# Kernel tuning notes

Hardware: AMD Instinct MI355X
Metric: run time of the kernel (lower is better)

Reference implementation:

```python
import jax, jax.numpy as jnp
import numpy as np

B, S, H, NH, HD = 2, 2048, 1024, 16, 64
THETA = 10000.0


def setup_inputs() -> dict:
    key = jax.random.key(0)
    k1, k2, k3, k4, k5 = jax.random.split(key, 5)
    hidden_states = jax.random.normal(k1, (B, S, H), dtype=jnp.float32)
    # RoPE tables, interleaved-pair layout: [c0,c0,c1,c1,...] along head_dim
    inv_freq = 1.0 / (THETA ** (jnp.arange(0, HD, 2, dtype=jnp.float32) / HD))
    t = jnp.arange(S, dtype=jnp.float32)
    freqs = jnp.outer(t, inv_freq)                      # [S, HD//2]
    freqs_cos = jnp.repeat(jnp.cos(freqs), 2, axis=-1)  # [S, HD]
    freqs_sin = jnp.repeat(jnp.sin(freqs), 2, axis=-1)  # [S, HD]
    position_ids = jnp.arange(S, dtype=jnp.int32)
    w = 0.02
    Wq = jax.random.normal(k2, (H, H), dtype=jnp.float32) * w
    Wk = jax.random.normal(k3, (H, H), dtype=jnp.float32) * w
    Wv = jax.random.normal(k4, (H, H), dtype=jnp.float32) * w
    Wo = jax.random.normal(k5, (H, H), dtype=jnp.float32) * w
    return {"hidden_states": hidden_states, "freqs_cos": freqs_cos,
            "freqs_sin": freqs_sin, "position_ids": position_ids,
            "Wq": Wq, "Wk": Wk, "Wv": Wv, "Wo": Wo}


def _rotate_half_interleaved(x):
    # stack([-x[..., 1::2], x[..., ::2]], -1).reshape_as(x)
    xe = x.reshape(x.shape[:-1] + (HD // 2, 2))
    return jnp.stack([-xe[..., 1], xe[..., 0]], axis=-1).reshape(x.shape)


def reference(hidden_states, freqs_cos, freqs_sin, position_ids, Wq, Wk, Wv, Wo):
    b, s, _ = hidden_states.shape
    # QKV projections (torch Linear: y = x @ W.T), split into heads [b, nh, s, hd]
    q = jnp.einsum('bsh,oh->bso', hidden_states, Wq).reshape(b, s, NH, HD).transpose(0, 2, 1, 3)
    k = jnp.einsum('bsh,oh->bso', hidden_states, Wk).reshape(b, s, NH, HD).transpose(0, 2, 1, 3)
    v = jnp.einsum('bsh,oh->bso', hidden_states, Wv).reshape(b, s, NH, HD).transpose(0, 2, 1, 3)
    cos = freqs_cos[position_ids][None, None]  # [1, 1, s, hd]
    sin = freqs_sin[position_ids][None, None]
    rq = _rotate_half_interleaved(q)
    # NOTE: faithful to source bug — rotate_half_k is built from q, not k
    q = q * cos + rq * sin
    k = k * cos + rq * sin
    # causal SDPA, scale = 1/sqrt(head_dim)
    scores = jnp.einsum('bhqd,bhkd->bhqk', q, k) / jnp.sqrt(jnp.float32(HD))
    causal = jnp.tril(jnp.ones((s, s), dtype=bool))
    scores = jnp.where(causal, scores, jnp.float32(-1e30))
    attn = jax.nn.softmax(scores, axis=-1)
    out = jnp.einsum('bhqk,bhkd->bhqd', attn, v)
    out = out.transpose(0, 2, 1, 3).reshape(b, s, H)
    return jnp.einsum('bsh,oh->bso', out, Wo)
```

## Files before the change

### kernel.cpp

```cpp
#include <hip/hip_runtime.h>
#include <stdint.h>

#define BB 2
#define SS 2048
#define HH 1024
#define NHH 16
#define HDD 64

typedef short bf16s;
typedef __attribute__((ext_vector_type(8))) short short8;
typedef __attribute__((ext_vector_type(4))) short short4v;
typedef __attribute__((ext_vector_type(2))) short short2v;
typedef __attribute__((ext_vector_type(4))) float f32x4;
typedef _Float16 half4v __attribute__((ext_vector_type(4)));
typedef _Float16 half8v __attribute__((ext_vector_type(8)));
typedef __fp16 fp16x2 __attribute__((ext_vector_type(2)));

__device__ inline short f2bf(float f) {
  union { float f; uint32_t u; } v; v.f = f;
  uint32_t r = (v.u + 0x7fffu + ((v.u >> 16) & 1u)) >> 16;
  return (short)r;
}
__device__ inline float bf2f(short h) {
  union { uint32_t u; float f; } v; v.u = ((uint32_t)(uint16_t)h) << 16;
  return v.f;
}

__device__ __forceinline__ float exp2_raw(float x) {
  float r;
  asm("v_exp_f32 %0, %1\n\ts_nop 0" : "=v"(r) : "v"(x));
  return r;
}

__device__ inline void gld_lds16(const void* g, void* l) {
  __builtin_amdgcn_global_load_lds((const __attribute__((address_space(1))) void*)g,
                                   (__attribute__((address_space(3))) void*)l, 16, 0, 0);
}

__device__ inline void stv(short* C, size_t i, float v) { C[i] = f2bf(v); }
__device__ inline void stv(float* C, size_t i, float v) { C[i] = v; }

__device__ inline f32x4 mfma_k32(short8 a, short8 b, f32x4 c) {
  return __builtin_amdgcn_mfma_f32_16x16x32_bf16(a, b, c, 0, 0, 0);
}
__device__ inline f32x4 mfma_k32(half8v a, half8v b, f32x4 c) {
  return __builtin_amdgcn_mfma_f32_16x16x32_f16(a, b, c, 0, 0, 0);
}
template <typename ET> struct ftr;
template <> struct ftr<short>     { using v8 = short8; };
template <> struct ftr<_Float16>  { using v8 = half8v; };

__global__ __launch_bounds__(256) void convert_all(
    const float* __restrict__ x, const float* __restrict__ Wq,
    const float* __restrict__ Wk, const float* __restrict__ Wv,
    const float* __restrict__ Wo, bf16s* __restrict__ xb,
    bf16s* __restrict__ wqkv, _Float16* __restrict__ wof) {
  const long M1 = 1024L * 1024L;
  long e = (long)(blockIdx.x * blockDim.x + threadIdx.x) * 4;
  if (e < 7 * M1) {
    const float* src; bf16s* dst;
    if (e < 4 * M1)      { src = x  + e;            dst = xb   + e; }
    else if (e < 5 * M1) { src = Wq + (e - 4 * M1); dst = wqkv + (e - 4 * M1); }
    else if (e < 6 * M1) { src = Wk + (e - 5 * M1); dst = wqkv + (e - 4 * M1); }
    else                 { src = Wv + (e - 6 * M1); dst = wqkv + (e - 4 * M1); }
    float4 v = *(const float4*)src;
    short4v o;
    o.x = f2bf(v.x); o.y = f2bf(v.y); o.z = f2bf(v.z); o.w = f2bf(v.w);
    *(short4v*)dst = o;
  } else {
    float4 v = *(const float4*)(Wo + (e - 7 * M1));
    half4v o;
    o.x = (_Float16)v.x; o.y = (_Float16)v.y;
    o.z = (_Float16)v.z; o.w = (_Float16)v.w;
    *(half4v*)(wof + (e - 7 * M1)) = o;
  }
}

template <typename ET, typename OT, int MT>
__global__ __launch_bounds__(256) void gemm_bt(
    const ET* __restrict__ A, const ET* __restrict__ Bm,
    OT* __restrict__ C, int K, int ldc) {
  using V8 = typename ftr<ET>::v8;
  __shared__ __align__(16) ET As[MT * 32 * 64];
  __shared__ __align__(16) ET Bs[128 * 64];
  const int tid = threadIdx.x;
  const int lane = tid & 63, w = tid >> 6;
  const int quad = lane >> 4, mcol = lane & 15;
  const int bm = blockIdx.y * (MT * 32), bn = blockIdx.x * 128;
  const int wm = (w >> 1) * (MT * 16), wn = (w & 1) * 64;
  f32x4 acc[MT][4] = {};
  const int nkt = K >> 6;
  for (int kt = 0; kt < nkt; ++kt) {
    __syncthreads();
#pragma unroll
    for (int i = 0; i < MT; ++i) {
      int seg = (i * 4 + w) * 512;
      int flat = seg + lane * 8;
      int row = flat >> 6;
      int cpos = (flat >> 3) & 7;
      int cs = cpos ^ (row & 7);
      gld_lds16(A + (size_t)(bm + row) * K + kt * 64 + cs * 8, &As[seg]);
    }
#pragma unroll
    for (int i = 0; i < 4; ++i) {
      int seg = (i * 4 + w) * 512;
      int flat = seg + lane * 8;
      int row = flat >> 6;
      int cpos = (flat >> 3) & 7;
      int cs = cpos ^ (row & 7);
      gld_lds16(Bm + (size_t)(bn + row) * K + kt * 64 + cs * 8, &Bs[seg]);
    }
    __syncthreads();
#pragma unroll
    for (int ks = 0; ks < 2; ++ks) {
      V8 af[MT], bf[4];
#pragma unroll
      for (int mt = 0; mt < MT; ++mt) {
        int row = wm + mt * 16 + mcol;
        int cs = (ks * 4 + quad) ^ (row & 7);
        af[mt] = *(const V8*)&As[row * 64 + cs * 8];
      }
#pragma unroll
      for (int nt = 0; nt < 4; ++nt) {
        int row = wn + nt * 16 + mcol;
        int cs = (ks * 4 + quad) ^ (row & 7);
        bf[nt] = *(const V8*)&Bs[row * 64 + cs * 8];
      }
#pragma unroll
      for (int mt = 0; mt < MT; ++mt)
#pragma unroll
        for (int nt = 0; nt < 4; ++nt)
          acc[mt][nt] = mfma_k32(af[mt], bf[nt], acc[mt][nt]);
    }
  }
#pragma unroll
  for (int mt = 0; mt < MT; ++mt)
#pragma unroll
    for (int nt = 0; nt < 4; ++nt) {
      int r0 = bm + wm + mt * 16 + quad * 4;
      int c = bn + wn + nt * 16 + mcol;
#pragma unroll
      for (int r = 0; r < 4; ++r)
        stv(C, (size_t)(r0 + r) * ldc + c, acc[mt][nt][r]);
    }
}

__global__ __launch_bounds__(256) void postproc(
    const bf16s* __restrict__ qkv, const float* __restrict__ fcos,
    const float* __restrict__ fsin, const int* __restrict__ pos,
    bf16s* __restrict__ Q, bf16s* __restrict__ Kc, _Float16* __restrict__ Vt) {
  const float LOG2E = 1.4426950408889634f;
  const int st = blockIdx.x, bh = blockIdx.y;
  const int b = bh >> 4, h = bh & 15;
  const int tid = threadIdx.x;
  const int m0 = b * 2048 + st * 64;
  {
    const int row = tid >> 2, pc = tid & 3;
    const int s = st * 64 + row;
    const int p = pos[s];
    const bf16s* qp = qkv + (size_t)(m0 + row) * 3072 + h * 64 + pc * 16;
    short8 qv[2] = { *(const short8*)qp, *(const short8*)(qp + 8) };
    short8 kv[2] = { *(const short8*)(qp + 1024), *(const short8*)(qp + 1032) };
    const float* cp = fcos + (size_t)p * 64 + pc * 16;
    const float* sp = fsin + (size_t)p * 64 + pc * 16;
    short8 qo[2], ko[2];
#pragma unroll
    for (int hf = 0; hf < 2; ++hf)
#pragma unroll
      for (int j = 0; j < 4; ++j) {
        float c = cp[hf * 8 + 2 * j], sn = sp[hf * 8 + 2 * j];
        float q0 = bf2f(qv[hf][2 * j]), q1 = bf2f(qv[hf][2 * j + 1]);
        float k0 = bf2f(kv[hf][2 * j]), k1 = bf2f(kv[hf][2 * j + 1]);
        qo[hf][2 * j]     = f2bf((q0 * c - q1 * sn) * 0.125f);
        qo[hf][2 * j + 1] = f2bf((q1 * c + q0 * sn) * 0.125f);
        ko[hf][2 * j]     = f2bf((k0 * c - q1 * sn) * LOG2E);
        ko[hf][2 * j + 1] = f2bf((k1 * c + q0 * sn) * LOG2E);
      }
    size_t o = ((size_t)bh * 2048 + s) * 64 + pc * 16;
    *(short8*)&Q[o] = qo[0];  *(short8*)&Q[o + 8] = qo[1];
    *(short8*)&Kc[o] = ko[0]; *(short8*)&Kc[o + 8] = ko[1];
  }
  __shared__ __align__(16) _Float16 T[64 * 72];
#pragma unroll
  for (int p2 = 0; p2 < 2; ++p2) {
    int sl = p2 * 32 + (tid >> 3);
    int ch = tid & 7;
    short8 v = *(const short8*)&qkv[(size_t)(m0 + sl) * 3072 + 2048 + h * 64 + ch * 8];
#pragma unroll
    for (int j = 0; j < 8; ++j) T[(ch * 8 + j) * 72 + sl] = (_Float16)bf2f(v[j]);
  }
  __syncthreads();
#pragma unroll
  for (int p2 = 0; p2 < 2; ++p2) {
    int dl = p2 * 32 + (tid >> 3);
    int ch = tid & 7;
    half8v v = *(const half8v*)&T[dl * 72 + ch * 8];
    *(half8v*)&Vt[((size_t)bh * 64 + dl) * 2048 + st * 64 + ch * 8] = v;
  }
}

template <bool DOB>
__device__ __forceinline__ void step2(
    const bf16s* __restrict__ Ks, const _Float16* __restrict__ Vp,
    const short8* bqA, const short8* bqB,
    f32x4* OA, f32x4* OB, float& lA, float& lB,
    bool diagA, bool diagB, int w, int quad, int col) {
  f32x4 sA[4], sB[4];
  __builtin_amdgcn_s_setprio(1);
#pragma unroll
  for (int t = 0; t < 4; ++t) {
    f32x4 a = {}, bb = {};
#pragma unroll
    for (int ks = 0; ks < 2; ++ks) {
      int krow = t * 16 + col;
      int cs = (ks * 4 + quad) ^ (krow & 7);
      short8 af = *(const short8*)&Ks[krow * 64 + cs * 8];
      a = __builtin_amdgcn_mfma_f32_16x16x32_bf16(af, bqA[ks], a, 0, 0, 0);
      if (DOB) bb = __builtin_amdgcn_mfma_f32_16x16x32_bf16(af, bqB[ks], bb, 0, 0, 0);
    }
    sA[t] = a;
    if (DOB) sB[t] = bb;
  }
  __builtin_amdgcn_s_setprio(0);
  if (diagA) {
#pragma unroll
    for (int t = 0; t < 4; ++t)
#pragma unroll
      for (int r = 0; r < 4; ++r)
        if (t * 16 + quad * 4 + r > w * 16 + col) sA[t][r] = -1e30f;
  }
  if (DOB && diagB) {
#pragma unroll
    for (int t = 0; t < 4; ++t)
#pragma unroll
      for (int r = 0; r < 4; ++r)
        if (t * 16 + quad * 4 + r > w * 16 + col) sB[t][r] = -1e30f;
  }
  half4v paA[4], paB[4];
#pragma unroll
  for (int t = 0; t < 4; ++t) {
    {
      float p0 = exp2_raw(sA[t][0]), p1 = exp2_raw(sA[t][1]);
      float p2 = exp2_raw(sA[t][2]), p3 = exp2_raw(sA[t][3]);
      lA += (p0 + p1) + (p2 + p3);
      union { fp16x2 h2[2]; half4v h4; } u;
      u.h2[0] = __builtin_amdgcn_cvt_pkrtz(p0, p1);
      u.h2[1] = __builtin_amdgcn_cvt_pkrtz(p2, p3);
      paA[t] = u.h4;
    }
    if (DOB) {
      float p0 = exp2_raw(sB[t][0]), p1 = exp2_raw(sB[t][1]);
      float p2 = exp2_raw(sB[t][2]), p3 = exp2_raw(sB[t][3]);
      lB += (p0 + p1) + (p2 + p3);
      union { fp16x2 h2[2]; half4v h4; } u;
      u.h2[0] = __builtin_amdgcn_cvt_pkrtz(p0, p1);
      u.h2[1] = __builtin_amdgcn_cvt_pkrtz(p2, p3);
      paB[t] = u.h4;
    }
  }
  __builtin_amdgcn_s_setprio(1);
#pragma unroll
  for (int dt = 0; dt < 4; ++dt) {
    int vrow = dt * 16 + col;
    const _Float16* vp = &Vp[vrow * 72 + (quad ^ (vrow & 3)) * 16];
    union { half8v v8; half4v v4[2]; } a01, a23;
    a01.v8 = *(const half8v*)vp;
    a23.v8 = *(const half8v*)(vp + 8);
    half4v bv[4] = { a01.v4[0], a01.v4[1], a23.v4[0], a23.v4[1] };
#pragma unroll
    for (int t = 0; t < 4; ++t) {
      OA[dt] = __builtin_amdgcn_mfma_f32_16x16x16f16(paA[t], bv[t], OA[dt], 0, 0, 0);
      if (DOB) OB[dt] = __builtin_amdgcn_mfma_f32_16x16x16f16(paB[t], bv[t], OB[dt], 0, 0, 0);
    }
  }
  __builtin_amdgcn_s_setprio(0);
}

__global__ __launch_bounds__(256) void attn(
    const bf16s* __restrict__ Q, const bf16s* __restrict__ Kb,
    const _Float16* __restrict__ Vt, _Float16* __restrict__ O) {
  __shared__ __align__(16) bf16s Ks[64 * 64];
  __shared__ __align__(16) _Float16 Vp[64 * 72];
  const int bh = blockIdx.y;
  const int tid = threadIdx.x, lane = tid & 63, w = tid >> 6;
  const int quad = lane >> 4, col = lane & 15;
  const size_t base = (size_t)bh * 2048 * 64;
  const _Float16* vbase = Vt + (size_t)bh * 64 * 2048;
  const int b = bh >> 4, h = bh & 15;
  const int x = blockIdx.x;
  const int qbA = 31 - x, qbB = x;

  short8 bqA[2], bqB[2];
  {
    const int qrA = qbA * 64 + w * 16 + col;
    const int qrB = qbB * 64 + w * 16 + col;
#pragma unroll
    for (int ks = 0; ks < 2; ++ks) {
      bqA[ks] = *(const short8*)&Q[base + (size_t)qrA * 64 + ks * 32 + quad * 8];
      bqB[ks] = *(const short8*)&Q[base + (size_t)qrB * 64 + ks * 32 + quad * 8];
    }
  }
  f32x4 OA[4] = {}, OB[4] = {};
  float lA = 0.f, lB = 0.f;

  const int vd = tid >> 2, vc = tid & 3;
  const int rot = vd & 3;
  for (int kt = 0; kt <= qbA; ++kt) {
    half8v vr0 = *(const half8v*)&vbase[(size_t)vd * 2048 + kt * 64 + vc * 16];
    half8v vr1 = *(const half8v*)&vbase[(size_t)vd * 2048 + kt * 64 + vc * 16 + 8];
    __syncthreads();
    {
      union { half8v v8; half4v v4[2]; } u0, u1;
      u0.v8 = vr0; u1.v8 = vr1;
      int rbase = vd * 72 + vc * 4;
      *(half4v*)&Vp[rbase + (0 ^ rot) * 16] = u0.v4[0];
      *(half4v*)&Vp[rbase + (1 ^ rot) * 16] = u0.v4[1];
      *(half4v*)&Vp[rbase + (2 ^ rot) * 16] = u1.v4[0];
      *(half4v*)&Vp[rbase + (3 ^ rot) * 16] = u1.v4[1];
    }
#pragma unroll
    for (int i = 0; i < 2; ++i) {
      int seg = (i * 4 + w) * 512;
      int flat = seg + lane * 8;
      int row = flat >> 6, cpos = (flat >> 3) & 7;
      int cs = cpos ^ (row & 7);
      gld_lds16(&Kb[base + (size_t)(kt * 64 + row) * 64 + cs * 8], &Ks[seg]);
    }
    __syncthreads();
    if (kt <= qbB)
      step2<true>(Ks, Vp, bqA, bqB, OA, OB, lA, lB,
                  false, kt == qbB, w, quad, col);
    else
      step2<false>(Ks, Vp, bqA, bqB, OA, OB, lA, lB,
                   kt == qbA, false, w, quad, col);
  }

  lA += __shfl_xor(lA, 16); lA += __shfl_xor(lA, 32);
  lB += __shfl_xor(lB, 16); lB += __shfl_xor(lB, 32);

#pragma unroll
  for (int which = 0; which < 2; ++which) {
    const int qb = which ? qbB : qbA;
    const f32x4* Oacc = which ? OB : OA;
    const float l = which ? lB : lA;
    float l4[4];
#pragma unroll
    for (int r = 0; r < 4; ++r) l4[r] = __shfl(l, quad * 4 + r);
#pragma unroll
    for (int dt = 0; dt < 4; ++dt)
#pragma unroll
      for (int r = 0; r < 4; ++r) {
        int srow = qb * 64 + w * 16 + quad * 4 + r;
        O[((size_t)b * 2048 + srow) * 1024 + h * 64 + dt * 16 + col] =
            (_Float16)(Oacc[dt][r] / l4[r]);
      }
  }
}

extern "C" void kernel_launch(void* const* d_in, const int* in_sizes, int n_in,
                              void* d_out, int out_size, void* d_ws, size_t ws_size,
                              hipStream_t stream) {
  (void)in_sizes; (void)n_in; (void)out_size; (void)ws_size;
  const float* x  = (const float*)d_in[0];
  const float* fc = (const float*)d_in[1];
  const float* fs = (const float*)d_in[2];
  const int* pos  = (const int*)d_in[3];
  const float* Wq = (const float*)d_in[4];
  const float* Wk = (const float*)d_in[5];
  const float* Wv = (const float*)d_in[6];
  const float* Wo = (const float*)d_in[7];
  float* out = (float*)d_out;
  char* ws = (char*)d_ws;
  const size_t MB = 1024 * 1024;
  bf16s* xb    = (bf16s*)(ws);
  bf16s* wqkv  = (bf16s*)(ws + 8 * MB);
  _Float16* wof = (_Float16*)(ws + 14 * MB);
  bf16s* qkv   = (bf16s*)(ws + 16 * MB);
  bf16s* Qb    = (bf16s*)(ws + 40 * MB);
  bf16s* Kb    = (bf16s*)(ws + 48 * MB);
  _Float16* Vt = (_Float16*)(ws + 56 * MB);
  _Float16* Ob = (_Float16*)(ws);

  convert_all<<<8192, 256, 0, stream>>>(x, Wq, Wk, Wv, Wo, xb, wqkv, wof);
  gemm_bt<short, short, 4><<<dim3(24, 32), 256, 0, stream>>>(xb, wqkv, qkv, 1024, 3072);
  postproc<<<dim3(32, 32), 256, 0, stream>>>(qkv, fc, fs, pos, Qb, Kb, Vt);
  attn<<<dim3(16, 32), 256, 0, stream>>>(Qb, Kb, Vt, Ob);
  gemm_bt<_Float16, float, 2><<<dim3(8, 64), 256, 0, stream>>>(Ob, wof, out, 1024, 1024);
}
```

Measured before the change: 196.8 us.

## Read K and V tiles directly from global memory instead of staging in LDS

Removes the shared-memory staging of K and V tiles and the two block barriers per key tile. Each wave now loads its MFMA operands for K and transposed V straight from global memory, which is expected to be served from L2 because all four waves read the same tile. This trades LDS traffic and synchronisation for four times the global/L2 load traffic and exposed load latency with no prefetch.

```diff
diff --git a/kernel.cpp b/kernel.cpp
--- a/kernel.cpp
+++ b/kernel.cpp
@@ -200,8 +200,8 @@
 }
 
 template <bool DOB>
-__device__ __forceinline__ void step2(
-    const bf16s* __restrict__ Ks, const _Float16* __restrict__ Vp,
+__device__ __forceinline__ void step2g(
+    const bf16s* __restrict__ Kg, const _Float16* __restrict__ Vg,
     const short8* bqA, const short8* bqB,
     f32x4* OA, f32x4* OB, float& lA, float& lB,
     bool diagA, bool diagB, int w, int quad, int col) {
@@ -212,9 +212,7 @@
     f32x4 a = {}, bb = {};
 #pragma unroll
     for (int ks = 0; ks < 2; ++ks) {
-      int krow = t * 16 + col;
-      int cs = (ks * 4 + quad) ^ (krow & 7);
-      short8 af = *(const short8*)&Ks[krow * 64 + cs * 8];
+      short8 af = *(const short8*)&Kg[(size_t)(t * 16 + col) * 64 + ks * 32 + quad * 8];
       a = __builtin_amdgcn_mfma_f32_16x16x32_bf16(af, bqA[ks], a, 0, 0, 0);
       if (DOB) bb = __builtin_amdgcn_mfma_f32_16x16x32_bf16(af, bqB[ks], bb, 0, 0, 0);
     }
@@ -222,6 +220,12 @@
     if (DOB) sB[t] = bb;
   }
   __builtin_amdgcn_s_setprio(0);
+  half4v bva[4][4];
+#pragma unroll
+  for (int dt = 0; dt < 4; ++dt)
+#pragma unroll
+    for (int t = 0; t < 4; ++t)
+      bva[dt][t] = *(const half4v*)&Vg[(size_t)(dt * 16 + col) * 2048 + t * 16 + quad * 4];
   if (diagA) {
 #pragma unroll
     for (int t = 0; t < 4; ++t)
@@ -261,16 +265,10 @@
   __builtin_amdgcn_s_setprio(1);
 #pragma unroll
   for (int dt = 0; dt < 4; ++dt) {
-    int vrow = dt * 16 + col;
-    const _Float16* vp = &Vp[vrow * 72 + (quad ^ (vrow & 3)) * 16];
-    union { half8v v8; half4v v4[2]; } a01, a23;
-    a01.v8 = *(const half8v*)vp;
-    a23.v8 = *(const half8v*)(vp + 8);
-    half4v bv[4] = { a01.v4[0], a01.v4[1], a23.v4[0], a23.v4[1] };
 #pragma unroll
     for (int t = 0; t < 4; ++t) {
-      OA[dt] = __builtin_amdgcn_mfma_f32_16x16x16f16(paA[t], bv[t], OA[dt], 0, 0, 0);
-      if (DOB) OB[dt] = __builtin_amdgcn_mfma_f32_16x16x16f16(paB[t], bv[t], OB[dt], 0, 0, 0);
+      OA[dt] = __builtin_amdgcn_mfma_f32_16x16x16f16(paA[t], bva[dt][t], OA[dt], 0, 0, 0);
+      if (DOB) OB[dt] = __builtin_amdgcn_mfma_f32_16x16x16f16(paB[t], bva[dt][t], OB[dt], 0, 0, 0);
     }
   }
   __builtin_amdgcn_s_setprio(0);
@@ -279,8 +277,6 @@
 __global__ __launch_bounds__(256) void attn(
     const bf16s* __restrict__ Q, const bf16s* __restrict__ Kb,
     const _Float16* __restrict__ Vt, _Float16* __restrict__ O) {
-  __shared__ __align__(16) bf16s Ks[64 * 64];
-  __shared__ __align__(16) _Float16 Vp[64 * 72];
   const int bh = blockIdx.y;
   const int tid = threadIdx.x, lane = tid & 63, w = tid >> 6;
   const int quad = lane >> 4, col = lane & 15;
@@ -303,36 +299,15 @@
   f32x4 OA[4] = {}, OB[4] = {};
   float lA = 0.f, lB = 0.f;
 
-  const int vd = tid >> 2, vc = tid & 3;
-  const int rot = vd & 3;
   for (int kt = 0; kt <= qbA; ++kt) {
-    half8v vr0 = *(const half8v*)&vbase[(size_t)vd * 2048 + kt * 64 + vc * 16];
-    half8v vr1 = *(const half8v*)&vbase[(size_t)vd * 2048 + kt * 64 + vc * 16 + 8];
-    __syncthreads();
-    {
-      union { half8v v8; half4v v4[2]; } u0, u1;
-      u0.v8 = vr0; u1.v8 = vr1;
-      int rbase = vd * 72 + vc * 4;
-      *(half4v*)&Vp[rbase + (0 ^ rot) * 16] = u0.v4[0];
-      *(half4v*)&Vp[rbase + (1 ^ rot) * 16] = u0.v4[1];
-      *(half4v*)&Vp[rbase + (2 ^ rot) * 16] = u1.v4[0];
-      *(half4v*)&Vp[rbase + (3 ^ rot) * 16] = u1.v4[1];
-    }
-#pragma unroll
-    for (int i = 0; i < 2; ++i) {
-      int seg = (i * 4 + w) * 512;
-      int flat = seg + lane * 8;
-      int row = flat >> 6, cpos = (flat >> 3) & 7;
-      int cs = cpos ^ (row & 7);
-      gld_lds16(&Kb[base + (size_t)(kt * 64 + row) * 64 + cs * 8], &Ks[seg]);
-    }
-    __syncthreads();
+    const bf16s* Kg = Kb + base + (size_t)kt * 64 * 64;
+    const _Float16* Vg = vbase + kt * 64;
     if (kt <= qbB)
-      step2<true>(Ks, Vp, bqA, bqB, OA, OB, lA, lB,
-                  false, kt == qbB, w, quad, col);
+      step2g<true>(Kg, Vg, bqA, bqB, OA, OB, lA, lB,
+                   false, kt == qbB, w, quad, col);
     else
-      step2<false>(Ks, Vp, bqA, bqB, OA, OB, lA, lB,
-                   kt == qbA, false, w, quad, col);
+      step2g<false>(Kg, Vg, bqA, bqB, OA, OB, lA, lB,
+                    kt == qbA, false, w, quad, col);
   }
 
   lA += __shfl_xor(lA, 16); lA += __shfl_xor(lA, 32);
```

Result: slower. 320.7 us (+63.0%).
